# Kernel tuning notes

Measured on AMD Instinct MI355X. Metric: run time of the kernel, lower is better.

Reference implementation:

```python
import jax, jax.numpy as jnp
import numpy as np
from jax import lax

C = 64

def _conv1x1(x, W):
    # x: [b,c,h,w], W: [o,c] (1x1 conv, no bias)
    return jnp.einsum('oc,bchw->bohw', W, x)

def _conv3x3(x, W):
    # x: [b,cin,h,w], W: [cout,cin,3,3], stride 1, pad 1, no bias
    return lax.conv_general_dilated(x, W, window_strides=(1, 1), padding='SAME',
                                    dimension_numbers=('NCHW', 'OIHW', 'NCHW'))


def setup_inputs() -> dict:
    key = jax.random.key(0)
    ks = jax.random.split(key, 12)
    b, c, h, w = 2, C, 320, 320
    s = 0.02
    inp = {
        'u': jax.random.normal(ks[0], (b, c, h, w), jnp.float32),
        'd': jax.random.normal(ks[1], (b, c, h, w), jnp.float32),
        'Wu1': jax.random.normal(ks[2], (c, c), jnp.float32) * s,
        'Wu2': jax.random.normal(ks[3], (c, c), jnp.float32) * s,
        'Wd1': jax.random.normal(ks[4], (c, c), jnp.float32) * s,
        'Wd2': jax.random.normal(ks[5], (c, c), jnp.float32) * s,
        'W1a': jax.random.normal(ks[6], (c, 2 * c, 3, 3), jnp.float32) * s,
        'W1b': jax.random.normal(ks[7], (c, c, 3, 3), jnp.float32) * s,
        'W2a': jax.random.normal(ks[8], (c, 2 * c, 3, 3), jnp.float32) * s,
        'W2b': jax.random.normal(ks[9], (c, c, 3, 3), jnp.float32) * s,
    }
    return inp


def reference(u, d, Wu1, Wu2, Wd1, Wd2, W1a, W1b, W2a, W2b):
    # 1x1 projections (torch permutes are absorbed into einsum subscripts)
    u1 = _conv1x1(u, Wu1)  # query for u->d attention
    u2 = _conv1x1(u, Wu2)  # key   for d->u attention
    d1 = _conv1x1(d, Wd1)  # query for d->u attention
    d2 = _conv1x1(d, Wd2)  # key   for u->d attention

    # per-row (axial over width) attention: scores [b,h,w_q,w_k]
    u_d = jax.nn.softmax(jnp.einsum('bchw,bchv->bhwv', u1, d2), axis=-1)
    d_u = jax.nn.softmax(jnp.einsum('bchw,bchv->bhwv', d1, u2), axis=-1)

    # attend over the raw opposite stream, back to NCHW
    buffer_d = jnp.einsum('bhwv,bchv->bchw', u_d, d)
    buffer_u = jnp.einsum('bhwv,bchv->bchw', d_u, u)

    out_u = _conv3x3(jax.nn.relu(_conv3x3(jnp.concatenate([u, buffer_d], axis=1), W1a)), W1b)
    out_d = _conv3x3(jax.nn.relu(_conv3x3(jnp.concatenate([d, buffer_u], axis=1), W2a)), W2b)
    return (out_u, out_d)
```

## Files before the change

kernel.cpp:

```cpp
#include <hip/hip_runtime.h>
#include <stdint.h>


typedef __bf16 bf16;
typedef __bf16 bf16x8 __attribute__((ext_vector_type(8)));
typedef float  f32x4  __attribute__((ext_vector_type(4)));

#define MFMA(a, b, c) __builtin_amdgcn_mfma_f32_16x16x32_bf16((a), (b), (c), 0, 0, 0)

static constexpr int    HWc  = 320 * 320;
static constexpr int    CHW  = 64 * HWc;
static constexpr size_t NE   = 2ull * CHW;

static constexpr size_t OFF_UBF  = 0;
static constexpr size_t OFF_DBF  = NE;
static constexpr size_t OFF_UT   = 2 * NE;
static constexpr size_t OFF_DT   = 3 * NE;
static constexpr size_t OFF_QUD  = 4 * NE;
static constexpr size_t OFF_KUD  = 5 * NE;
static constexpr size_t OFF_QDU  = 6 * NE;
static constexpr size_t OFF_KDU  = 7 * NE;
static constexpr size_t OFF_BUFD = 8 * NE;
static constexpr size_t OFF_BUFU = 9 * NE;
static constexpr size_t OFF_W1A  = 10 * NE;
static constexpr size_t OFF_W2A  = OFF_W1A + 9*64*128;
static constexpr size_t OFF_W1B  = OFF_W2A + 9*64*128;
static constexpr size_t OFF_W2B  = OFF_W1B + 9*64*64;
static constexpr size_t OFF_WU1  = OFF_W2B + 9*64*64;
static constexpr size_t OFF_WU2  = OFF_WU1 + 4096;
static constexpr size_t OFF_WD1  = OFF_WU2 + 4096;
static constexpr size_t OFF_WD2  = OFF_WD1 + 4096;

__global__ __launch_bounds__(256) void kpack(
    const float* __restrict__ Wu1, const float* __restrict__ Wu2,
    const float* __restrict__ Wd1, const float* __restrict__ Wd2,
    const float* __restrict__ W1a, const float* __restrict__ W1b,
    const float* __restrict__ W2a, const float* __restrict__ W2b,
    bf16* __restrict__ ws) {
  const int t = blockIdx.x * 256 + threadIdx.x;
  if (t < 9 * 64 * 128) {
    const int c = t & 127, o = (t >> 7) & 63, tap = t >> 13;
    const int src = (o * 128 + c) * 9 + tap;
    ws[OFF_W1A + t] = (bf16)W1a[src];
    ws[OFF_W2A + t] = (bf16)W2a[src];
  }
  if (t < 9 * 64 * 64) {
    const int c = t & 63, o = (t >> 6) & 63, tap = t >> 12;
    const int src = (o * 64 + c) * 9 + tap;
    ws[OFF_W1B + t] = (bf16)W1b[src];
    ws[OFF_W2B + t] = (bf16)W2b[src];
  }
  if (t < 4096) {
    ws[OFF_WU1 + t] = (bf16)Wu1[t];
    ws[OFF_WU2 + t] = (bf16)Wu2[t];
    ws[OFF_WD1 + t] = (bf16)Wd1[t];
    ws[OFF_WD2 + t] = (bf16)Wd2[t];
  }
}

__global__ __launch_bounds__(256) void kproj(const float* __restrict__ u,
                                             const float* __restrict__ d,
                                             bf16* __restrict__ ws) {
  __shared__ float ut[64][68];
  __shared__ float stg[4][16][68];
  const int s   = blockIdx.z;
  const int by  = blockIdx.y;
  const int b   = by / 320;
  const int y   = by % 320;
  const int x0  = blockIdx.x * 64;
  const int tid = threadIdx.x;
  const int lane = tid & 63, wv = tid >> 6;
  const int l15 = lane & 15, q4 = lane >> 4;

  const float* src = s ? d : u;
  const bf16* Wq = ws + (s ? OFF_WD1 : OFF_WU1);
  const bf16* Wk = ws + (s ? OFF_WD2 : OFF_WU2);
  bf16* xbf = ws + (s ? OFF_DBF : OFF_UBF);
  bf16* xt  = ws + (s ? OFF_DT  : OFF_UT);
  bf16* qo  = ws + (s ? OFF_QDU : OFF_QUD);
  bf16* ko  = ws + (s ? OFF_KUD : OFF_KDU);

  {
    const int xl = lane;
    const int cb = wv * 16;
#pragma unroll
    for (int i = 0; i < 16; ++i) {
      const int c = cb + i;
      const size_t g = (size_t)(b * 64 + c) * HWc + (size_t)y * 320 + x0 + xl;
      const float v = src[g];
      xbf[g] = (bf16)v;
      ut[xl][c] = v;
    }
  }
  __syncthreads();

  {
    const int xl = tid >> 2;
    const int cc = (tid & 3) * 16;
    bf16x8 v0, v1;
#pragma unroll
    for (int j = 0; j < 8; ++j) {
      v0[j] = (bf16)ut[xl][cc + j];
      v1[j] = (bf16)ut[xl][cc + 8 + j];
    }
    bf16* p = xt + ((size_t)by * 320 + x0 + xl) * 64 + cc;
    *(bf16x8*)p = v0;
    *(bf16x8*)(p + 8) = v1;
  }

  bf16x8 a[2];
#pragma unroll
  for (int ks = 0; ks < 2; ++ks) {
    const int xl = wv * 16 + l15;
    const int c0 = ks * 32 + q4 * 8;
#pragma unroll
    for (int j = 0; j < 8; ++j) a[ks][j] = (bf16)ut[xl][c0 + j];
  }
  const f32x4 zero4 = {0.f, 0.f, 0.f, 0.f};
  f32x4 acc[8];
#pragma unroll
  for (int i = 0; i < 8; ++i) acc[i] = zero4;
#pragma unroll
  for (int ks = 0; ks < 2; ++ks) {
#pragma unroll
    for (int ot = 0; ot < 8; ++ot) {
      const bf16* Wm = (ot < 4) ? Wq : Wk;
      const int o = (ot & 3) * 16 + l15;
      const bf16x8 bw = *(const bf16x8*)(Wm + o * 64 + ks * 32 + q4 * 8);
      acc[ot] = MFMA(a[ks], bw, acc[ot]);
    }
  }
#pragma unroll
  for (int pass = 0; pass < 2; ++pass) {
    bf16* dst = pass ? ko : qo;
#pragma unroll
    for (int ot = 0; ot < 4; ++ot)
#pragma unroll
      for (int r = 0; r < 4; ++r)
        stg[wv][q4 * 4 + r][ot * 16 + l15] = acc[pass * 4 + ot][r];
    bf16x8 v0, v1;
    const int cc = q4 * 16;
#pragma unroll
    for (int j = 0; j < 8; ++j) {
      v0[j] = (bf16)stg[wv][l15][cc + j];
      v1[j] = (bf16)stg[wv][l15][cc + 8 + j];
    }
    bf16* p = dst + ((size_t)by * 320 + x0 + wv * 16 + l15) * 64 + cc;
    *(bf16x8*)p = v0;
    *(bf16x8*)(p + 8) = v1;
  }
}

__global__ __launch_bounds__(256) void kattn(bf16* __restrict__ ws) {
  __shared__ __attribute__((aligned(16))) bf16 ksh[20480];
  __shared__ __attribute__((aligned(16))) bf16 pch[4][16][72];
  const int bh  = blockIdx.x;
  const int dir = blockIdx.y;
  const int t5  = blockIdx.z;
  const int tid = threadIdx.x;
  const int lane = tid & 63, wv = tid >> 6;
  const int l15 = lane & 15, q4 = lane >> 4;

  const bf16* Q = ws + (dir ? OFF_QDU : OFF_QUD) + (size_t)bh * 320 * 64;
  const bf16* K = ws + (dir ? OFF_KDU : OFF_KUD) + (size_t)bh * 320 * 64;
  const bf16* V = ws + (dir ? OFF_UBF : OFF_DBF) + (size_t)(bh / 320) * CHW
                + (size_t)(bh % 320) * 320;
  bf16* O = ws + (dir ? OFF_BUFU : OFF_BUFD) + (size_t)bh * 320 * 64;

  for (int i = tid; i < 2560; i += 256) {
    const int px = i >> 3, s = i & 7;
    const int t = px >> 4, r = px & 15;
    *(bf16x8*)(ksh + t * 1024 + s * 128 + r * 8) =
        *(const bf16x8*)(K + (size_t)px * 64 + s * 8);
  }
  __syncthreads();

  const f32x4 zero4 = {0.f, 0.f, 0.f, 0.f};
  const int wq0 = (t5 * 4 + wv) * 16;
  const bf16x8 a0 = *(const bf16x8*)(Q + (size_t)(wq0 + l15) * 64 + q4 * 8);
  const bf16x8 a1 = *(const bf16x8*)(Q + (size_t)(wq0 + l15) * 64 + 32 + q4 * 8);
  f32x4 sacc[20];
#pragma unroll
  for (int kt = 0; kt < 20; ++kt) sacc[kt] = zero4;
#pragma unroll
  for (int kt = 0; kt < 20; ++kt) {
    const bf16x8 b0 = *(const bf16x8*)(ksh + kt * 1024 + q4 * 128 + l15 * 8);
    const bf16x8 b1 = *(const bf16x8*)(ksh + kt * 1024 + (q4 + 4) * 128 + l15 * 8);
    sacc[kt] = MFMA(a0, b0, sacc[kt]);
    sacc[kt] = MFMA(a1, b1, sacc[kt]);
  }
  float mx[4] = {-3.0e38f, -3.0e38f, -3.0e38f, -3.0e38f};
#pragma unroll
  for (int kt = 0; kt < 20; ++kt)
#pragma unroll
    for (int r = 0; r < 4; ++r) mx[r] = fmaxf(mx[r], sacc[kt][r]);
#pragma unroll
  for (int off = 1; off < 16; off <<= 1)
#pragma unroll
    for (int r = 0; r < 4; ++r) mx[r] = fmaxf(mx[r], __shfl_xor(mx[r], off));
  float sm[4] = {0.f, 0.f, 0.f, 0.f};
#pragma unroll
  for (int kt = 0; kt < 20; ++kt)
#pragma unroll
    for (int r = 0; r < 4; ++r) {
      const float e = __expf(sacc[kt][r] - mx[r]);
      sacc[kt][r] = e;
      sm[r] += e;
    }
#pragma unroll
  for (int off = 1; off < 16; off <<= 1)
#pragma unroll
    for (int r = 0; r < 4; ++r) sm[r] += __shfl_xor(sm[r], off);
  float inv[4];
#pragma unroll
  for (int r = 0; r < 4; ++r) inv[r] = 1.f / sm[r];

  f32x4 oac[4];
#pragma unroll
  for (int ct = 0; ct < 4; ++ct) oac[ct] = zero4;
#pragma unroll
  for (int ch = 0; ch < 5; ++ch) {
#pragma unroll
    for (int j = 0; j < 4; ++j) {
      const int kt = ch * 4 + j;
#pragma unroll
      for (int r = 0; r < 4; ++r)
        pch[wv][q4 * 4 + r][j * 16 + l15] = (bf16)(sacc[kt][r] * inv[r]);
    }
    const bf16x8 p0 = *(const bf16x8*)&pch[wv][l15][q4 * 8];
    const bf16x8 p1 = *(const bf16x8*)&pch[wv][l15][32 + q4 * 8];
#pragma unroll
    for (int ct = 0; ct < 4; ++ct) {
      const bf16* vp = V + (size_t)(ct * 16 + l15) * HWc + ch * 64 + q4 * 8;
      const bf16x8 v0 = *(const bf16x8*)vp;
      const bf16x8 v1 = *(const bf16x8*)(vp + 32);
      oac[ct] = MFMA(p0, v0, oac[ct]);
      oac[ct] = MFMA(p1, v1, oac[ct]);
    }
  }
#pragma unroll
  for (int ct = 0; ct < 4; ++ct)
#pragma unroll
    for (int r = 0; r < 4; ++r)
      pch[wv][q4 * 4 + r][ct * 16 + l15] = (bf16)oac[ct][r];
  __builtin_amdgcn_s_waitcnt(0);
  bf16x8 w0, w1;
  const int cc = q4 * 16;
#pragma unroll
  for (int j = 0; j < 8; ++j) {
    w0[j] = pch[wv][l15][cc + j];
    w1[j] = pch[wv][l15][cc + 8 + j];
  }
  bf16* p = O + (size_t)(wq0 + l15) * 64 + cc;
  *(bf16x8*)p = w0;
  *(bf16x8*)(p + 8) = w1;
}

__global__ __launch_bounds__(256, 3) void kconv1(bf16* __restrict__ ws) {
  __shared__ __attribute__((aligned(16))) bf16 xs[10 * 8 * 34 * 8];
  __shared__ __attribute__((aligned(16))) bf16 stg[4][16][72];
  const int s = blockIdx.z >> 1, b = blockIdx.z & 1;
  const int x0 = blockIdx.x * 32;
  const int y0 = blockIdx.y * 8;
  const int tid = threadIdx.x;
  const int lane = tid & 63, wv = tid >> 6;
  const int l15 = lane & 15, q4 = lane >> 4;

  const bf16* X1 = ws + (s ? OFF_DT : OFF_UT) + (size_t)b * CHW;
  const bf16* X2 = ws + (s ? OFF_BUFU : OFF_BUFD) + (size_t)b * CHW;
  const bf16* Wg = ws + (s ? OFF_W2A : OFF_W1A);
  bf16* Mo = ws + (s ? OFF_QDU : OFF_QUD) + (size_t)b * CHW;

  const f32x4 zero4 = {0.f, 0.f, 0.f, 0.f};
  f32x4 acc[2][2][4];
#pragma unroll
  for (int r = 0; r < 2; ++r)
#pragma unroll
    for (int xt = 0; xt < 2; ++xt)
#pragma unroll
      for (int ot = 0; ot < 4; ++ot) acc[r][xt][ot] = zero4;

  for (int t = 0; t < 2; ++t) {
    __syncthreads();
    const bf16* Xt = t ? X2 : X1;
    for (int i = tid; i < 2720; i += 256) {
      const int row = i / 272, rem = i % 272;
      const int px = rem >> 3, chunk = rem & 7;
      const int yy = y0 - 1 + row, xx = x0 - 1 + px;
      bf16x8 v;
#pragma unroll
      for (int j = 0; j < 8; ++j) v[j] = (bf16)0.f;
      if ((unsigned)yy < 320u && (unsigned)xx < 320u)
        v = *(const bf16x8*)(Xt + ((size_t)yy * 320 + xx) * 64 + chunk * 8);
      *(bf16x8*)(xs + (((row * 8 + chunk) * 34 + px) * 8)) = v;
    }
    __syncthreads();
#pragma unroll
    for (int ky = 0; ky < 3; ++ky)
#pragma unroll
      for (int kx = 0; kx < 3; ++kx)
#pragma unroll
        for (int ks = 0; ks < 2; ++ks) {
          const int tap = ky * 3 + kx;
          bf16x8 bw[4];
#pragma unroll
          for (int ot = 0; ot < 4; ++ot)
            bw[ot] = *(const bf16x8*)(Wg + ((size_t)tap * 64 + ot * 16 + l15) * 128
                                      + t * 64 + ks * 32 + q4 * 8);
          bf16x8 af[2][2];
#pragma unroll
          for (int r = 0; r < 2; ++r)
#pragma unroll
            for (int xt = 0; xt < 2; ++xt)
              af[r][xt] = *(const bf16x8*)(xs + (((wv * 2 + r + ky) * 8 + ks * 4 + q4) * 34
                                                 + xt * 16 + l15 + kx) * 8);
#pragma unroll
          for (int r = 0; r < 2; ++r)
#pragma unroll
            for (int xt = 0; xt < 2; ++xt)
#pragma unroll
              for (int ot = 0; ot < 4; ++ot)
                acc[r][xt][ot] = MFMA(af[r][xt], bw[ot], acc[r][xt][ot]);
        }
  }
#pragma unroll
  for (int r = 0; r < 2; ++r)
#pragma unroll
    for (int xt = 0; xt < 2; ++xt) {
#pragma unroll
      for (int ot = 0; ot < 4; ++ot)
#pragma unroll
        for (int rr = 0; rr < 4; ++rr)
          stg[wv][q4 * 4 + rr][ot * 16 + l15] = (bf16)fmaxf(acc[r][xt][ot][rr], 0.f);
      __builtin_amdgcn_s_waitcnt(0);
      bf16x8 w0, w1;
      const int cc = q4 * 16;
#pragma unroll
      for (int j = 0; j < 8; ++j) {
        w0[j] = stg[wv][l15][cc + j];
        w1[j] = stg[wv][l15][cc + 8 + j];
      }
      const int y = y0 + wv * 2 + r;
      bf16* p = Mo + ((size_t)y * 320 + x0 + xt * 16 + l15) * 64 + cc;
      *(bf16x8*)p = w0;
      *(bf16x8*)(p + 8) = w1;
    }
}

__global__ __launch_bounds__(256, 3) void kconv2(const bf16* __restrict__ ws,
                                                 float* __restrict__ out) {
  __shared__ __attribute__((aligned(16))) bf16 xs[10 * 8 * 34 * 8];
  const int s = blockIdx.z >> 1, b = blockIdx.z & 1;
  const int x0 = blockIdx.x * 32;
  const int y0 = blockIdx.y * 8;
  const int tid = threadIdx.x;
  const int lane = tid & 63, wv = tid >> 6;
  const int l15 = lane & 15, q4 = lane >> 4;

  const bf16* X  = ws + (s ? OFF_QDU : OFF_QUD) + (size_t)b * CHW;
  const bf16* Wg = ws + (s ? OFF_W2B : OFF_W1B);
  float* O = out + (size_t)s * NE + (size_t)b * CHW;

  const f32x4 zero4 = {0.f, 0.f, 0.f, 0.f};
  f32x4 acc[2][2][4];
#pragma unroll
  for (int r = 0; r < 2; ++r)
#pragma unroll
    for (int xt = 0; xt < 2; ++xt)
#pragma unroll
      for (int ot = 0; ot < 4; ++ot) acc[r][xt][ot] = zero4;

  for (int i = tid; i < 2720; i += 256) {
    const int row = i / 272, rem = i % 272;
    const int px = rem >> 3, chunk = rem & 7;
    const int yy = y0 - 1 + row, xx = x0 - 1 + px;
    bf16x8 v;
#pragma unroll
    for (int j = 0; j < 8; ++j) v[j] = (bf16)0.f;
    if ((unsigned)yy < 320u && (unsigned)xx < 320u)
      v = *(const bf16x8*)(X + ((size_t)yy * 320 + xx) * 64 + chunk * 8);
    *(bf16x8*)(xs + (((row * 8 + chunk) * 34 + px) * 8)) = v;
  }
  __syncthreads();
#pragma unroll
  for (int ky = 0; ky < 3; ++ky)
#pragma unroll
    for (int kx = 0; kx < 3; ++kx)
#pragma unroll
      for (int ks = 0; ks < 2; ++ks) {
        const int tap = ky * 3 + kx;
        bf16x8 bw[4];
#pragma unroll
        for (int ot = 0; ot < 4; ++ot)
          bw[ot] = *(const bf16x8*)(Wg + ((size_t)tap * 64 + ot * 16 + l15) * 64
                                    + ks * 32 + q4 * 8);
        bf16x8 af[2][2];
#pragma unroll
        for (int r = 0; r < 2; ++r)
#pragma unroll
          for (int xt = 0; xt < 2; ++xt)
            af[r][xt] = *(const bf16x8*)(xs + (((wv * 2 + r + ky) * 8 + ks * 4 + q4) * 34
                                               + xt * 16 + l15 + kx) * 8);
#pragma unroll
        for (int r = 0; r < 2; ++r)
#pragma unroll
          for (int xt = 0; xt < 2; ++xt)
#pragma unroll
            for (int ot = 0; ot < 4; ++ot)
              acc[r][xt][ot] = MFMA(af[r][xt], bw[ot], acc[r][xt][ot]);
      }
#pragma unroll
  for (int r = 0; r < 2; ++r)
#pragma unroll
    for (int xt = 0; xt < 2; ++xt)
#pragma unroll
      for (int ot = 0; ot < 4; ++ot) {
        const int o = ot * 16 + l15;
        const int y = y0 + wv * 2 + r;
        float* p = O + (size_t)o * HWc + (size_t)y * 320 + x0 + xt * 16 + q4 * 4;
        *(f32x4*)p = acc[r][xt][ot];
      }
}

extern "C" void kernel_launch(void* const* d_in, const int* in_sizes, int n_in,
                              void* d_out, int out_size, void* d_ws, size_t ws_size,
                              hipStream_t stream) {
  const float* u   = (const float*)d_in[0];
  const float* d   = (const float*)d_in[1];
  const float* Wu1 = (const float*)d_in[2];
  const float* Wu2 = (const float*)d_in[3];
  const float* Wd1 = (const float*)d_in[4];
  const float* Wd2 = (const float*)d_in[5];
  const float* W1a = (const float*)d_in[6];
  const float* W1b = (const float*)d_in[7];
  const float* W2a = (const float*)d_in[8];
  const float* W2b = (const float*)d_in[9];
  bf16* ws = (bf16*)d_ws;
  float* out = (float*)d_out;

  kpack<<<dim3((9 * 64 * 128 + 255) / 256), 256, 0, stream>>>(
      Wu1, Wu2, Wd1, Wd2, W1a, W1b, W2a, W2b, ws);
  kproj<<<dim3(5, 640, 2), 256, 0, stream>>>(u, d, ws);
  kattn<<<dim3(640, 2, 5), 256, 0, stream>>>(ws);
  kconv1<<<dim3(10, 40, 4), 256, 0, stream>>>(ws);
  kconv2<<<dim3(10, 40, 4), 256, 0, stream>>>(ws, out);
}
```

Before: 724.8 us.

## Split conv input tiles into two 16-column halves to shrink LDS and raise occupancy

Both 3x3 conv kernels now stage the input halo in two 18-column halves instead of one 34-column tile, roughly halving the shared-memory buffer. Launch bounds go from 3 to 4 blocks per CU. The change aims to fit more resident waves so global-load latency is better hidden. In exchange, each half reloads its 2-column overlap, adds a barrier per phase, and the shared weight fragments are loaded twice as often.

```diff
diff --git a/kernel.cpp b/kernel.cpp
--- a/kernel.cpp
+++ b/kernel.cpp
@@ -256,8 +256,8 @@
   *(bf16x8*)(p + 8) = w1;
 }
 
-__global__ __launch_bounds__(256, 3) void kconv1(bf16* __restrict__ ws) {
-  __shared__ __attribute__((aligned(16))) bf16 xs[10 * 8 * 34 * 8];
+__global__ __launch_bounds__(256, 4) void kconv1(bf16* __restrict__ ws) {
+  __shared__ __attribute__((aligned(16))) bf16 xs[10 * 8 * 18 * 8];
   __shared__ __attribute__((aligned(16))) bf16 stg[4][16][72];
   const int s = blockIdx.z >> 1, b = blockIdx.z & 1;
   const int x0 = blockIdx.x * 32;
@@ -276,23 +276,26 @@
 #pragma unroll
   for (int r = 0; r < 2; ++r)
 #pragma unroll
-    for (int xt = 0; xt < 2; ++xt)
-#pragma unroll
-      for (int ot = 0; ot < 4; ++ot) acc[r][xt][ot] = zero4;
-
-  for (int t = 0; t < 2; ++t) {
-    __syncthreads();
+    for (int xh = 0; xh < 2; ++xh)
+#pragma unroll
+      for (int ot = 0; ot < 4; ++ot) acc[r][xh][ot] = zero4;
+
+  for (int ph = 0; ph < 4; ++ph) {
+    const int t = ph >> 1, xh = ph & 1;
     const bf16* Xt = t ? X2 : X1;
-    for (int i = tid; i < 2720; i += 256) {
-      const int row = i / 272, rem = i % 272;
-      const int px = rem >> 3, chunk = rem & 7;
-      const int yy = y0 - 1 + row, xx = x0 - 1 + px;
+    const int xbase = x0 + xh * 16 - 1;
+    if (ph) __syncthreads();
+    for (int i = tid; i < 1440; i += 256) {
+      const int chunk = i & 7;
+      const int px = (i >> 3) % 18;
+      const int row = i / 144;
+      const int yy = y0 - 1 + row, xx = xbase + px;
       bf16x8 v;
 #pragma unroll
       for (int j = 0; j < 8; ++j) v[j] = (bf16)0.f;
       if ((unsigned)yy < 320u && (unsigned)xx < 320u)
         v = *(const bf16x8*)(Xt + ((size_t)yy * 320 + xx) * 64 + chunk * 8);
-      *(bf16x8*)(xs + (((row * 8 + chunk) * 34 + px) * 8)) = v;
+      *(bf16x8*)(xs + (((row * 8 + chunk) * 18 + px) * 8)) = v;
     }
     __syncthreads();
 #pragma unroll
@@ -307,31 +310,27 @@
           for (int ot = 0; ot < 4; ++ot)
             bw[ot] = *(const bf16x8*)(Wg + ((size_t)tap * 64 + ot * 16 + l15) * 128
                                       + t * 64 + ks * 32 + q4 * 8);
-          bf16x8 af[2][2];
+          bf16x8 af[2];
 #pragma unroll
           for (int r = 0; r < 2; ++r)
-#pragma unroll
-            for (int xt = 0; xt < 2; ++xt)
-              af[r][xt] = *(const bf16x8*)(xs + (((wv * 2 + r + ky) * 8 + ks * 4 + q4) * 34
-                                                 + xt * 16 + l15 + kx) * 8);
+            af[r] = *(const bf16x8*)(xs + (((wv * 2 + r + ky) * 8 + ks * 4 + q4) * 18
+                                           + l15 + kx) * 8);
 #pragma unroll
           for (int r = 0; r < 2; ++r)
 #pragma unroll
-            for (int xt = 0; xt < 2; ++xt)
-#pragma unroll
-              for (int ot = 0; ot < 4; ++ot)
-                acc[r][xt][ot] = MFMA(af[r][xt], bw[ot], acc[r][xt][ot]);
+            for (int ot = 0; ot < 4; ++ot)
+              acc[r][xh][ot] = MFMA(af[r], bw[ot], acc[r][xh][ot]);
         }
   }
 #pragma unroll
   for (int r = 0; r < 2; ++r)
 #pragma unroll
-    for (int xt = 0; xt < 2; ++xt) {
+    for (int xh = 0; xh < 2; ++xh) {
 #pragma unroll
       for (int ot = 0; ot < 4; ++ot)
 #pragma unroll
         for (int rr = 0; rr < 4; ++rr)
-          stg[wv][q4 * 4 + rr][ot * 16 + l15] = (bf16)fmaxf(acc[r][xt][ot][rr], 0.f);
+          stg[wv][q4 * 4 + rr][ot * 16 + l15] = (bf16)fmaxf(acc[r][xh][ot][rr], 0.f);
       __builtin_amdgcn_s_waitcnt(0);
       bf16x8 w0, w1;
       const int cc = q4 * 16;
@@ -341,15 +340,15 @@
         w1[j] = stg[wv][l15][cc + 8 + j];
       }
       const int y = y0 + wv * 2 + r;
-      bf16* p = Mo + ((size_t)y * 320 + x0 + xt * 16 + l15) * 64 + cc;
+      bf16* p = Mo + ((size_t)y * 320 + x0 + xh * 16 + l15) * 64 + cc;
       *(bf16x8*)p = w0;
       *(bf16x8*)(p + 8) = w1;
     }
 }
 
-__global__ __launch_bounds__(256, 3) void kconv2(const bf16* __restrict__ ws,
+__global__ __launch_bounds__(256, 4) void kconv2(const bf16* __restrict__ ws,
                                                  float* __restrict__ out) {
-  __shared__ __attribute__((aligned(16))) bf16 xs[10 * 8 * 34 * 8];
+  __shared__ __attribute__((aligned(16))) bf16 xs[10 * 8 * 18 * 8];
   const int s = blockIdx.z >> 1, b = blockIdx.z & 1;
   const int x0 = blockIdx.x * 32;
   const int y0 = blockIdx.y * 8;
@@ -366,59 +365,60 @@
 #pragma unroll
   for (int r = 0; r < 2; ++r)
 #pragma unroll
-    for (int xt = 0; xt < 2; ++xt)
-#pragma unroll
-      for (int ot = 0; ot < 4; ++ot) acc[r][xt][ot] = zero4;
-
-  for (int i = tid; i < 2720; i += 256) {
-    const int row = i / 272, rem = i % 272;
-    const int px = rem >> 3, chunk = rem & 7;
-    const int yy = y0 - 1 + row, xx = x0 - 1 + px;
-    bf16x8 v;
-#pragma unroll
-    for (int j = 0; j < 8; ++j) v[j] = (bf16)0.f;
-    if ((unsigned)yy < 320u && (unsigned)xx < 320u)
-      v = *(const bf16x8*)(X + ((size_t)yy * 320 + xx) * 64 + chunk * 8);
-    *(bf16x8*)(xs + (((row * 8 + chunk) * 34 + px) * 8)) = v;
-  }
-  __syncthreads();
-#pragma unroll
-  for (int ky = 0; ky < 3; ++ky)
-#pragma unroll
-    for (int kx = 0; kx < 3; ++kx)
-#pragma unroll
-      for (int ks = 0; ks < 2; ++ks) {
-        const int tap = ky * 3 + kx;
-        bf16x8 bw[4];
-#pragma unroll
-        for (int ot = 0; ot < 4; ++ot)
-          bw[ot] = *(const bf16x8*)(Wg + ((size_t)tap * 64 + ot * 16 + l15) * 64
-                                    + ks * 32 + q4 * 8);
-        bf16x8 af[2][2];
-#pragma unroll
-        for (int r = 0; r < 2; ++r)
-#pragma unroll
-          for (int xt = 0; xt < 2; ++xt)
-            af[r][xt] = *(const bf16x8*)(xs + (((wv * 2 + r + ky) * 8 + ks * 4 + q4) * 34
-                                               + xt * 16 + l15 + kx) * 8);
-#pragma unroll
-        for (int r = 0; r < 2; ++r)
-#pragma unroll
-          for (int xt = 0; xt < 2; ++xt)
+    for (int xh = 0; xh < 2; ++xh)
+#pragma unroll
+      for (int ot = 0; ot < 4; ++ot) acc[r][xh][ot] = zero4;
+
+  for (int xh = 0; xh < 2; ++xh) {
+    const int xbase = x0 + xh * 16 - 1;
+    if (xh) __syncthreads();
+    for (int i = tid; i < 1440; i += 256) {
+      const int chunk = i & 7;
+      const int px = (i >> 3) % 18;
+      const int row = i / 144;
+      const int yy = y0 - 1 + row, xx = xbase + px;
+      bf16x8 v;
+#pragma unroll
+      for (int j = 0; j < 8; ++j) v[j] = (bf16)0.f;
+      if ((unsigned)yy < 320u && (unsigned)xx < 320u)
+        v = *(const bf16x8*)(X + ((size_t)yy * 320 + xx) * 64 + chunk * 8);
+      *(bf16x8*)(xs + (((row * 8 + chunk) * 18 + px) * 8)) = v;
+    }
+    __syncthreads();
+#pragma unroll
+    for (int ky = 0; ky < 3; ++ky)
+#pragma unroll
+      for (int kx = 0; kx < 3; ++kx)
+#pragma unroll
+        for (int ks = 0; ks < 2; ++ks) {
+          const int tap = ky * 3 + kx;
+          bf16x8 bw[4];
+#pragma unroll
+          for (int ot = 0; ot < 4; ++ot)
+            bw[ot] = *(const bf16x8*)(Wg + ((size_t)tap * 64 + ot * 16 + l15) * 64
+                                      + ks * 32 + q4 * 8);
+          bf16x8 af[2];
+#pragma unroll
+          for (int r = 0; r < 2; ++r)
+            af[r] = *(const bf16x8*)(xs + (((wv * 2 + r + ky) * 8 + ks * 4 + q4) * 18
+                                           + l15 + kx) * 8);
+#pragma unroll
+          for (int r = 0; r < 2; ++r)
 #pragma unroll
             for (int ot = 0; ot < 4; ++ot)
-              acc[r][xt][ot] = MFMA(af[r][xt], bw[ot], acc[r][xt][ot]);
-      }
+              acc[r][xh][ot] = MFMA(af[r], bw[ot], acc[r][xh][ot]);
+        }
+  }
 #pragma unroll
   for (int r = 0; r < 2; ++r)
 #pragma unroll
-    for (int xt = 0; xt < 2; ++xt)
+    for (int xh = 0; xh < 2; ++xh)
 #pragma unroll
       for (int ot = 0; ot < 4; ++ot) {
         const int o = ot * 16 + l15;
         const int y = y0 + wv * 2 + r;
-        float* p = O + (size_t)o * HWc + (size_t)y * 320 + x0 + xt * 16 + q4 * 4;
-        *(f32x4*)p = acc[r][xt][ot];
+        float* p = O + (size_t)o * HWc + (size_t)y * 320 + x0 + xh * 16 + q4 * 4;
+        *(f32x4*)p = acc[r][xh][ot];
       }
 }
 
```

Result: slower. 1.150 ms (+58.7%).
